# Kernel optimization log

Measured on AMD Instinct MI355X. Metric: run time of the kernel, lower is better.

Reference implementation:

```python
import jax, jax.numpy as jnp
import numpy as np

P = 2048
D = 1024
H = 16
DH = D // H
HID = 32


def setup_inputs() -> dict:
    key = jax.random.key(0)
    ks = jax.random.split(key, 10)
    s = 0.02
    return {
        "x": jax.random.normal(ks[0], (P, D), jnp.float32),
        "rel": jax.random.normal(ks[1], (P, P, 2), jnp.float32),
        "w_qkv": jax.random.normal(ks[2], (D, 3 * D), jnp.float32) * s,
        "w_proj": jax.random.normal(ks[3], (D, D), jnp.float32) * s,
        "rpb_w1": jax.random.normal(ks[4], (2, HID), jnp.float32) * s,
        "rpb_b1": jnp.zeros((HID,), jnp.float32),
        "rpb_w2": jax.random.normal(ks[5], (HID, HID), jnp.float32) * s,
        "rpb_b2": jnp.zeros((HID,), jnp.float32),
        "rpb_w3": jax.random.normal(ks[6], (HID, 1), jnp.float32) * s,
        "rpb_b3": jnp.zeros((1,), jnp.float32),
    }


def reference(x, rel, w_qkv, w_proj, rpb_w1, rpb_b1, rpb_w2, rpb_b2, rpb_w3, rpb_b3):
    scale = 1.0 / np.sqrt(DH)
    qkv = x @ w_qkv                                   # [P, 3D]
    q, k, v = jnp.split(qkv, 3, axis=-1)
    # [P, D] -> [H, P, DH]
    q = q.reshape(P, H, DH).transpose(1, 0, 2)
    k = k.reshape(P, H, DH).transpose(1, 0, 2)
    v = v.reshape(P, H, DH).transpose(1, 0, 2)
    logits = jnp.einsum('hpd,hqd->hpq', q, k) * scale  # [H, P, P]
    # RelPosBias MLP: (dx,dy) -> scalar, applied over [P, P, 2]
    hcur = jax.nn.relu(rel @ rpb_w1 + rpb_b1)
    hcur = jax.nn.relu(hcur @ rpb_w2 + rpb_b2)
    bias = (hcur @ rpb_w3 + rpb_b3)[..., 0]            # [P, P]
    logits = logits + bias[None]
    attn = jax.nn.softmax(logits, axis=-1)
    out = jnp.einsum('hpq,hqd->hpd', attn, v)          # [H, P, DH]
    out = out.transpose(1, 0, 2).reshape(P, D)
    return out @ w_proj
```

## Files before the change

### kernel.cpp

```cpp
#include <hip/hip_runtime.h>
#include <hip/hip_bf16.h>
#include <type_traits>

typedef __attribute__((ext_vector_type(8))) short bf16x8;
typedef __attribute__((ext_vector_type(4))) float floatx4;
typedef __attribute__((ext_vector_type(2))) float float2v;

__device__ __forceinline__ float bf2f(unsigned short u) {
    union { unsigned int x; float f; } v; v.x = ((unsigned int)u) << 16; return v.f;
}
__device__ __forceinline__ unsigned short f2bf(float f) {
    union { float f; unsigned int u; } v; v.f = f;
    unsigned int x = v.u;
    unsigned int r = x + 0x7fffu + ((x >> 16) & 1u);
    return (unsigned short)(r >> 16);
}

typedef const __attribute__((address_space(1))) unsigned int u32_g;
typedef __attribute__((address_space(3))) unsigned int u32_l;
__device__ __forceinline__ void gld_lds16(const void* g, void* l) {
    __builtin_amdgcn_global_load_lds((u32_g*)g, (u32_l*)l, 16, 0, 0);
}

__device__ __forceinline__ void trans32(const float* __restrict__ in,
                                        unsigned short* __restrict__ out,
                                        int K, int N, int bx, int by,
                                        unsigned short (*T)[33]) {
    const int n0 = bx * 32, k0 = by * 32;
    const int r = threadIdx.x >> 3;
    const int c4 = (threadIdx.x & 7) * 4;
    float4 v = *reinterpret_cast<const float4*>(in + (size_t)(k0 + r) * N + n0 + c4);
    T[c4 + 0][r] = f2bf(v.x);
    T[c4 + 1][r] = f2bf(v.y);
    T[c4 + 2][r] = f2bf(v.z);
    T[c4 + 3][r] = f2bf(v.w);
    __syncthreads();
    ushort4 o = {T[r][c4], T[r][c4 + 1], T[r][c4 + 2], T[r][c4 + 3]};
    *reinterpret_cast<ushort4*>(out + (size_t)(n0 + r) * K + k0 + c4) = o;
}

__global__ __launch_bounds__(256) void prep(const float* __restrict__ x,
                                            unsigned short* __restrict__ xb,
                                            const float* __restrict__ wq,
                                            unsigned short* __restrict__ wqT,
                                            const float* __restrict__ wp,
                                            unsigned short* __restrict__ wpT) {
    __shared__ unsigned short T[32][33];
    const int b = blockIdx.x;
    if (b < 1024) {
        size_t i = ((size_t)b * 256 + threadIdx.x) * 8;
        float4 a = *reinterpret_cast<const float4*>(x + i);
        float4 c = *reinterpret_cast<const float4*>(x + i + 4);
        unsigned short t[8] = {f2bf(a.x), f2bf(a.y), f2bf(a.z), f2bf(a.w),
                               f2bf(c.x), f2bf(c.y), f2bf(c.z), f2bf(c.w)};
        *reinterpret_cast<uint4*>(xb + i) = *reinterpret_cast<const uint4*>(t);
    } else if (b < 4096) {
        int t = b - 1024;
        trans32(wq, wqT, 1024, 3072, t % 96, t / 96, T);
    } else {
        int t = b - 4096;
        trans32(wp, wpT, 1024, 1024, t % 32, t / 32, T);
    }
}

__device__ __forceinline__ void gemm128_body(const unsigned short* __restrict__ A,
                                             const unsigned short* __restrict__ Bt,
                                             unsigned short* __restrict__ C,
                                             int bx, int by,
                                             unsigned short* __restrict__ S) {
    const int tid = threadIdx.x;
    const int wave = tid >> 6;
    const int lane = tid & 63;
    const int m15 = lane & 15;
    const int quad = lane >> 4;
    const int wm = wave >> 1;
    const int wn = wave & 1;
    const int m0 = by * 128;
    const int n0 = bx * 128;
    const int srow = lane >> 2;
    const int scol = (lane & 3) * 8;

    floatx4 acc[4][4];
#pragma unroll
    for (int mt = 0; mt < 4; mt++)
#pragma unroll
        for (int nt = 0; nt < 4; nt++) acc[mt][nt] = {0.f, 0.f, 0.f, 0.f};

    auto stage = [&](int k0, unsigned short* As, unsigned short* Bs) {
#pragma unroll
        for (int i = 0; i < 2; i++) {
            int j = wave * 2 + i;
            gld_lds16(A + (size_t)(m0 + j * 16 + srow) * 1024 + k0 + scol, &As[j * 16 * 32]);
            gld_lds16(Bt + (size_t)(n0 + j * 16 + srow) * 1024 + k0 + scol, &Bs[j * 16 * 32]);
        }
    };

    stage(0, S, S + 4096);
    __syncthreads();

    for (int kk = 0; kk < 32; ++kk) {
        unsigned short* As = S + (kk & 1) * 8192;
        unsigned short* Bs = As + 4096;
        if (kk < 31) {
            unsigned short* An = S + ((kk & 1) ^ 1) * 8192;
            stage((kk + 1) * 32, An, An + 4096);
        }

        bf16x8 a[4];
#pragma unroll
        for (int mt = 0; mt < 4; mt++)
            a[mt] = *reinterpret_cast<bf16x8*>(&As[(wm * 64 + mt * 16 + m15) * 32 + quad * 8]);
#pragma unroll
        for (int nt = 0; nt < 4; nt++) {
            bf16x8 b = *reinterpret_cast<bf16x8*>(&Bs[(wn * 64 + nt * 16 + m15) * 32 + quad * 8]);
#pragma unroll
            for (int mt = 0; mt < 4; mt++)
                acc[mt][nt] = __builtin_amdgcn_mfma_f32_16x16x32_bf16(a[mt], b, acc[mt][nt], 0, 0, 0);
        }
        __syncthreads();
    }

#pragma unroll
    for (int mt = 0; mt < 4; mt++)
#pragma unroll
        for (int nt = 0; nt < 4; nt++)
#pragma unroll
            for (int i = 0; i < 4; i++) {
                int row = m0 + wm * 64 + mt * 16 + quad * 4 + i;
                int col = n0 + wn * 64 + nt * 16 + m15;
                C[(size_t)row * 3072 + col] = f2bf(acc[mt][nt][i]);
            }
}

__device__ __forceinline__ void rpb_body(int bx,
                                         const float* __restrict__ rel,
                                         const float* __restrict__ w1,
                                         const float* __restrict__ b1,
                                         const float* __restrict__ w2,
                                         const float* __restrict__ b2,
                                         const float* __restrict__ w3,
                                         const float* __restrict__ b3,
                                         unsigned short* __restrict__ biasb) {
    const int tid = threadIdx.x;
    const int wave = tid >> 6;
    const int lane = tid & 63;
    const int m15 = lane & 15;
    const int quad = lane >> 4;

    bf16x8 af0, af1;
    {
        unsigned short t0[8], t1[8];
#pragma unroll
        for (int j = 0; j < 8; j++) {
            int k = quad * 8 + j;
            t0[j] = f2bf(w2[k * 32 + m15]);
            t1[j] = f2bf(w2[k * 32 + 16 + m15]);
        }
        af0 = *reinterpret_cast<bf16x8*>(t0);
        af1 = *reinterpret_cast<bf16x8*>(t1);
    }

    float2v w1a2[4], w1b2[4], b12[4];
#pragma unroll
    for (int p = 0; p < 4; p++) {
        int base = quad * 8 + 2 * p;
        w1a2[p] = {w1[base], w1[base + 1]};
        w1b2[p] = {w1[32 + base], w1[32 + base + 1]};
        b12[p]  = {b1[base], b1[base + 1]};
    }

    floatx4 b2r0, b2r1;
    float2v w3p00, w3p01, w3p10, w3p11;
    const float LOG2E = 1.44269504f;
    {
        float4 t0 = *reinterpret_cast<const float4*>(b2 + quad * 4);
        float4 t1 = *reinterpret_cast<const float4*>(b2 + 16 + quad * 4);
        b2r0 = {t0.x, t0.y, t0.z, t0.w};
        b2r1 = {t1.x, t1.y, t1.z, t1.w};
        float4 u0 = *reinterpret_cast<const float4*>(w3 + quad * 4);
        float4 u1 = *reinterpret_cast<const float4*>(w3 + 16 + quad * 4);
        w3p00 = {u0.x * LOG2E, u0.y * LOG2E};
        w3p01 = {u0.z * LOG2E, u0.w * LOG2E};
        w3p10 = {u1.x * LOG2E, u1.y * LOG2E};
        w3p11 = {u1.z * LOG2E, u1.w * LOG2E};
    }
    const float b3s = b3[0] * LOG2E;
    const float2v z2 = {0.f, 0.f};
    const floatx4 b3r = {b3s, b3s, b3s, b3s};

    bf16x8 sel;
    {
        unsigned short t[8];
#pragma unroll
        for (int j = 0; j < 8; j++)
            t[j] = (m15 == j) ? (unsigned short)0x3f80u : (unsigned short)0;
        sel = *reinterpret_cast<bf16x8*>(t);
    }

    const int base = bx * 1024 + wave * 64;

    float2 cur[4];
#pragma unroll
    for (int t = 0; t < 4; t++)
        cur[t] = *reinterpret_cast<const float2*>(rel + (size_t)(base + t * 16 + m15) * 2);

    for (int it = 0; it < 4; ++it) {
        const int pix0 = base + it * 256;
        float2 nxt[4];
        if (it < 3) {
#pragma unroll
            for (int t = 0; t < 4; t++)
                nxt[t] = *reinterpret_cast<const float2*>(rel + (size_t)(pix0 + 256 + t * 16 + m15) * 2);
        }

        float sreg[4];
#pragma unroll
        for (int t = 0; t < 4; t++) {
            float2v dx2 = {cur[t].x, cur[t].x}, dy2 = {cur[t].y, cur[t].y};

            unsigned int hp[4];
#pragma unroll
            for (int p = 0; p < 4; p++) {
                float2v h = __builtin_elementwise_fma(dx2, w1a2[p],
                             __builtin_elementwise_fma(dy2, w1b2[p], b12[p]));
                h = __builtin_elementwise_max(h, z2);
                hp[p] = __builtin_amdgcn_perm(__float_as_uint(h.y), __float_as_uint(h.x), 0x07060302u);
            }
            bf16x8 hb = *reinterpret_cast<bf16x8*>(hp);

            floatx4 d0 = __builtin_amdgcn_mfma_f32_16x16x32_bf16(af0, hb, b2r0, 0, 0, 0);
            floatx4 d1 = __builtin_amdgcn_mfma_f32_16x16x32_bf16(af1, hb, b2r1, 0, 0, 0);

            float2v m00 = __builtin_elementwise_max(__builtin_shufflevector(d0, d0, 0, 1), z2);
            float2v m01 = __builtin_elementwise_max(__builtin_shufflevector(d0, d0, 2, 3), z2);
            float2v m10 = __builtin_elementwise_max(__builtin_shufflevector(d1, d1, 0, 1), z2);
            float2v m11 = __builtin_elementwise_max(__builtin_shufflevector(d1, d1, 2, 3), z2);
            float2v acc2 = m00 * w3p00;
            acc2 = __builtin_elementwise_fma(m01, w3p01, acc2);
            acc2 = __builtin_elementwise_fma(m10, w3p10, acc2);
            acc2 = __builtin_elementwise_fma(m11, w3p11, acc2);
            sreg[t] = acc2.x + acc2.y;
        }

        unsigned int sb[4];
        sb[0] = (unsigned int)f2bf(sreg[0]) | ((unsigned int)f2bf(sreg[1]) << 16);
        sb[1] = (unsigned int)f2bf(sreg[2]) | ((unsigned int)f2bf(sreg[3]) << 16);
        sb[2] = 0; sb[3] = 0;
        bf16x8 sf = *reinterpret_cast<bf16x8*>(sb);
        floatx4 dsum = __builtin_amdgcn_mfma_f32_16x16x32_bf16(sel, sf, b3r, 0, 0, 0);

        if (quad == 0) {
            unsigned short o[4] = {f2bf(dsum[0]), f2bf(dsum[1]), f2bf(dsum[2]), f2bf(dsum[3])};
            *reinterpret_cast<ushort4*>(biasb + (size_t)pix0 + m15 * 4) =
                *reinterpret_cast<const ushort4*>(o);
        }

        if (it < 3) {
#pragma unroll
            for (int t = 0; t < 4; t++) cur[t] = nxt[t];
        }
    }
}

__global__ __launch_bounds__(256) void gemm_rpb(const unsigned short* __restrict__ xb,
                                                const unsigned short* __restrict__ wqT,
                                                unsigned short* __restrict__ qkv,
                                                const float* __restrict__ rel,
                                                const float* __restrict__ w1,
                                                const float* __restrict__ b1,
                                                const float* __restrict__ w2,
                                                const float* __restrict__ b2,
                                                const float* __restrict__ w3,
                                                const float* __restrict__ b3,
                                                unsigned short* __restrict__ biasb) {
    __shared__ __align__(16) unsigned short S[4 * 128 * 32];
    const int b = blockIdx.x;
    if (b < 384)
        gemm128_body(xb, wqT, qkv, b % 24, b / 24, S);
    else
        rpb_body(b - 384, rel, w1, b1, w2, b2, w3, b3, biasb);
}

template<int BN, typename TC>
__global__ __launch_bounds__(256) void gemm_abt(const unsigned short* __restrict__ A,
                                                const unsigned short* __restrict__ Bt,
                                                TC* __restrict__ C,
                                                int M, int N, int K) {
    constexpr int NT = BN / 32;
    __shared__ __align__(16) unsigned short As[2][64 * 32];
    __shared__ __align__(16) unsigned short Bs[2][BN * 32];

    const int tid = threadIdx.x;
    const int wave = tid >> 6;
    const int lane = tid & 63;
    const int m15 = lane & 15;
    const int quad = lane >> 4;
    const int wm = wave >> 1;
    const int wn = wave & 1;
    const int m0 = blockIdx.y * 64;
    const int n0 = blockIdx.x * BN;

    const int srow = lane >> 2;
    const int scol = (lane & 3) * 8;

    floatx4 acc[2][NT];
#pragma unroll
    for (int mt = 0; mt < 2; mt++)
#pragma unroll
        for (int nt = 0; nt < NT; nt++) acc[mt][nt] = {0.f, 0.f, 0.f, 0.f};

    auto stage = [&](int k0, int buf) {
        gld_lds16(A + (size_t)(m0 + wave * 16 + srow) * K + k0 + scol, &As[buf][wave * 16 * 32]);
#pragma unroll
        for (int i = 0; i < BN / 64; i++) {
            int j = wave * (BN / 64) + i;
            gld_lds16(Bt + (size_t)(n0 + j * 16 + srow) * K + k0 + scol, &Bs[buf][j * 16 * 32]);
        }
    };

    const int nk = K >> 5;
    stage(0, 0);
    __syncthreads();

    for (int kk = 0; kk < nk; ++kk) {
        const int cur = kk & 1;
        if (kk + 1 < nk) stage((kk + 1) * 32, cur ^ 1);

        bf16x8 a[2];
#pragma unroll
        for (int mt = 0; mt < 2; mt++)
            a[mt] = *reinterpret_cast<bf16x8*>(&As[cur][(wm * 32 + mt * 16 + m15) * 32 + quad * 8]);
#pragma unroll
        for (int nt = 0; nt < NT; nt++) {
            bf16x8 b = *reinterpret_cast<bf16x8*>(&Bs[cur][(wn * (BN / 2) + nt * 16 + m15) * 32 + quad * 8]);
#pragma unroll
            for (int mt = 0; mt < 2; mt++)
                acc[mt][nt] = __builtin_amdgcn_mfma_f32_16x16x32_bf16(a[mt], b, acc[mt][nt], 0, 0, 0);
        }
        __syncthreads();
    }

#pragma unroll
    for (int mt = 0; mt < 2; mt++)
#pragma unroll
        for (int nt = 0; nt < NT; nt++)
#pragma unroll
            for (int i = 0; i < 4; i++) {
                int row = m0 + wm * 32 + mt * 16 + quad * 4 + i;
                int col = n0 + wn * (BN / 2) + nt * 16 + m15;
                if constexpr (std::is_same<TC, float>::value)
                    C[(size_t)row * N + col] = acc[mt][nt][i];
                else
                    C[(size_t)row * N + col] = f2bf(acc[mt][nt][i]);
            }
}

__global__ __launch_bounds__(512, 4) void attn_kernel(const unsigned short* __restrict__ qkv,
                                                      const unsigned short* __restrict__ biasb,
                                                      unsigned short* __restrict__ attn_out) {
    const int h = blockIdx.x;
    const int q0 = blockIdx.y * 64;
    __shared__ __align__(16) unsigned short Kst[2][64 * 72];
    __shared__ __align__(16) unsigned short Vst[2][64 * 72];
    __shared__ __align__(16) unsigned short Ps[8][16 * 72];

    const int tid = threadIdx.x;
    const int g = tid >> 8;
    const int w = (tid >> 6) & 3;
    const int lane = tid & 63;
    const int ltid = tid & 255;
    const int m15 = lane & 15;
    const int quad = lane >> 4;

    bf16x8 qf[2];
#pragma unroll
    for (int kh = 0; kh < 2; kh++)
        qf[kh] = *reinterpret_cast<const bf16x8*>(
            qkv + (size_t)(q0 + w * 16 + m15) * 3072 + h * 64 + kh * 32 + quad * 8);

    const int kr0 = ltid >> 3, kd0 = (ltid & 7) * 8;
    const int ka = (ltid & 31) * 2;
    const int vd0 = (ltid >> 5) * 8;

    unsigned short* Kc = Kst[g];
    unsigned short* Vc = Vst[g];
    const size_t kofs = (size_t)g * 1024;

    uint4 kreg0 = *reinterpret_cast<const uint4*>(qkv + (kofs + kr0) * 3072 + 1024 + h * 64 + kd0);
    uint4 kreg1 = *reinterpret_cast<const uint4*>(qkv + (kofs + kr0 + 32) * 3072 + 1024 + h * 64 + kd0);
    uint4 vrega = *reinterpret_cast<const uint4*>(qkv + (kofs + ka) * 3072 + 2048 + h * 64 + vd0);
    uint4 vregb = *reinterpret_cast<const uint4*>(qkv + (kofs + ka + 1) * 3072 + 2048 + h * 64 + vd0);

    unsigned short br[16];
#pragma unroll
    for (int i = 0; i < 4; i++) {
        ushort4 t = *reinterpret_cast<const ushort4*>(
            biasb + (size_t)(q0 + w * 16 + quad * 4 + i) * 2048 + kofs + m15 * 4);
        br[0 * 4 + i] = t.x; br[1 * 4 + i] = t.y; br[2 * 4 + i] = t.z; br[3 * 4 + i] = t.w;
    }

    float rs[4] = {0.f, 0.f, 0.f, 0.f};
    floatx4 acc[4];
#pragma unroll
    for (int i = 0; i < 4; i++) acc[i] = {0.f, 0.f, 0.f, 0.f};
    const float c1 = 0.125f * 1.44269504f;

    for (int kt = 0; kt < 16; ++kt) {
        __syncthreads();

        *reinterpret_cast<uint4*>(&Kc[kr0 * 72 + kd0]) = kreg0;
        *reinterpret_cast<uint4*>(&Kc[(kr0 + 32) * 72 + kd0]) = kreg1;
        {
            const unsigned int* aw = reinterpret_cast<const unsigned int*>(&vrega);
            const unsigned int* bw = reinterpret_cast<const unsigned int*>(&vregb);
#pragma unroll
            for (int wd = 0; wd < 4; wd++) {
                unsigned int lo = __builtin_amdgcn_perm(bw[wd], aw[wd], 0x05040100u);
                unsigned int hi = __builtin_amdgcn_perm(bw[wd], aw[wd], 0x07060302u);
                *reinterpret_cast<unsigned int*>(&Vc[(vd0 + 2 * wd) * 72 + ka]) = lo;
                *reinterpret_cast<unsigned int*>(&Vc[(vd0 + 2 * wd + 1) * 72 + ka]) = hi;
            }
        }
        __syncthreads();

        if (kt < 15) {
            const size_t kb = kofs + (size_t)(kt + 1) * 64;
            kreg0 = *reinterpret_cast<const uint4*>(qkv + (kb + kr0) * 3072 + 1024 + h * 64 + kd0);
            kreg1 = *reinterpret_cast<const uint4*>(qkv + (kb + kr0 + 32) * 3072 + 1024 + h * 64 + kd0);
            vrega = *reinterpret_cast<const uint4*>(qkv + (kb + ka) * 3072 + 2048 + h * 64 + vd0);
            vregb = *reinterpret_cast<const uint4*>(qkv + (kb + ka + 1) * 3072 + 2048 + h * 64 + vd0);
        }

        floatx4 s[4];
#pragma unroll
        for (int nt = 0; nt < 4; nt++) s[nt] = {0.f, 0.f, 0.f, 0.f};
        __builtin_amdgcn_s_setprio(1);
#pragma unroll
        for (int kh = 0; kh < 2; kh++) {
#pragma unroll
            for (int nt = 0; nt < 4; nt++) {
                bf16x8 b = *reinterpret_cast<bf16x8*>(&Kc[(nt * 16 + m15) * 72 + kh * 32 + quad * 8]);
                s[nt] = __builtin_amdgcn_mfma_f32_16x16x32_bf16(qf[kh], b, s[nt], 0, 0, 0);
            }
        }
        __builtin_amdgcn_s_setprio(0);

        float p[4][4];
#pragma unroll
        for (int nt = 0; nt < 4; nt++)
#pragma unroll
            for (int i = 0; i < 4; i++) {
                float lg = fmaf(s[nt][i], c1, bf2f(br[nt * 4 + i]));
                p[nt][i] = __builtin_amdgcn_exp2f(lg);
                rs[i] += p[nt][i];
            }

        if (kt < 15) {
            const size_t kb = kofs + (size_t)(kt + 1) * 64;
#pragma unroll
            for (int i = 0; i < 4; i++) {
                ushort4 t = *reinterpret_cast<const ushort4*>(
                    biasb + (size_t)(q0 + w * 16 + quad * 4 + i) * 2048 + kb + m15 * 4);
                br[0 * 4 + i] = t.x; br[1 * 4 + i] = t.y; br[2 * 4 + i] = t.z; br[3 * 4 + i] = t.w;
            }
        }

        unsigned short* Pw = Ps[tid >> 6];
#pragma unroll
        for (int nt = 0; nt < 4; nt++)
#pragma unroll
            for (int i = 0; i < 4; i++)
                Pw[(quad * 4 + i) * 72 + nt * 16 + m15] = f2bf(p[nt][i]);
        __asm__ volatile("s_waitcnt lgkmcnt(0)" ::: "memory");

        __builtin_amdgcn_s_setprio(1);
#pragma unroll
        for (int kh = 0; kh < 2; kh++) {
            bf16x8 a = *reinterpret_cast<bf16x8*>(&Pw[m15 * 72 + kh * 32 + quad * 8]);
#pragma unroll
            for (int nt = 0; nt < 4; nt++) {
                bf16x8 b = *reinterpret_cast<bf16x8*>(&Vc[(nt * 16 + m15) * 72 + kh * 32 + quad * 8]);
                acc[nt] = __builtin_amdgcn_mfma_f32_16x16x32_bf16(a, b, acc[nt], 0, 0, 0);
            }
        }
        __builtin_amdgcn_s_setprio(0);
    }

    float rsum[4];
#pragma unroll
    for (int i = 0; i < 4; i++) {
        float r = rs[i];
        r += __shfl_xor(r, 1);
        r += __shfl_xor(r, 2);
        r += __shfl_xor(r, 4);
        r += __shfl_xor(r, 8);
        rsum[i] = r;
    }

    float* accbuf = reinterpret_cast<float*>(&Kst[0][0]);
    float* lbuf = accbuf + 4096;

    __syncthreads();
    if (g == 1) {
#pragma unroll
        for (int nt = 0; nt < 4; nt++)
#pragma unroll
            for (int i = 0; i < 4; i++)
                accbuf[(w * 16 + quad * 4 + i) * 64 + nt * 16 + m15] = acc[nt][i];
        if (m15 == 0) {
#pragma unroll
            for (int i = 0; i < 4; i++) lbuf[w * 16 + quad * 4 + i] = rsum[i];
        }
    }
    __syncthreads();
    if (g == 0) {
        float linv[4];
#pragma unroll
        for (int i = 0; i < 4; i++)
            linv[i] = 1.f / (rsum[i] + lbuf[w * 16 + quad * 4 + i]);
#pragma unroll
        for (int nt = 0; nt < 4; nt++)
#pragma unroll
            for (int i = 0; i < 4; i++) {
                float o = (acc[nt][i] + accbuf[(w * 16 + quad * 4 + i) * 64 + nt * 16 + m15]) * linv[i];
                int row = q0 + w * 16 + quad * 4 + i;
                int col = h * 64 + nt * 16 + m15;
                attn_out[(size_t)row * 1024 + col] = f2bf(o);
            }
    }
}

extern "C" void kernel_launch(void* const* d_in, const int* in_sizes, int n_in,
                              void* d_out, int out_size, void* d_ws, size_t ws_size,
                              hipStream_t stream) {
    const float* x      = (const float*)d_in[0];
    const float* rel    = (const float*)d_in[1];
    const float* w_qkv  = (const float*)d_in[2];
    const float* w_proj = (const float*)d_in[3];
    const float* w1     = (const float*)d_in[4];
    const float* b1     = (const float*)d_in[5];
    const float* w2     = (const float*)d_in[6];
    const float* b2     = (const float*)d_in[7];
    const float* w3     = (const float*)d_in[8];
    const float* b3     = (const float*)d_in[9];

    char* ws = (char*)d_ws;
    unsigned short* qkv   = (unsigned short*)ws;
    unsigned short* biasb = (unsigned short*)(ws + 12582912);
    unsigned short* xb    = (unsigned short*)(ws + 20971520);
    unsigned short* attn  = xb;
    unsigned short* wqT   = (unsigned short*)(ws + 25165824);
    unsigned short* wpT   = (unsigned short*)(ws + 31457280);
    float* out = (float*)d_out;

    prep<<<5120, 256, 0, stream>>>(x, xb, w_qkv, wqT, w_proj, wpT);
    gemm_rpb<<<4480, 256, 0, stream>>>(xb, wqT, qkv, rel, w1, b1, w2, b2, w3, b3, biasb);
    attn_kernel<<<dim3(16, 32), 512, 0, stream>>>(qkv, biasb, attn);
    gemm_abt<64, float><<<dim3(16, 32), 256, 0, stream>>>(attn, wpT, out, 2048, 1024, 1024);
}
```

Measured before the change: 208.8 us.

## Move RPB MLP into prep kernel and XOR-swizzle GEMM LDS tiles

```diff
diff --git a/kernel.cpp b/kernel.cpp
--- a/kernel.cpp
+++ b/kernel.cpp
@@ -39,27 +39,165 @@
     *reinterpret_cast<ushort4*>(out + (size_t)(n0 + r) * K + k0 + c4) = o;
 }
 
-__global__ __launch_bounds__(256) void prep(const float* __restrict__ x,
-                                            unsigned short* __restrict__ xb,
-                                            const float* __restrict__ wq,
-                                            unsigned short* __restrict__ wqT,
-                                            const float* __restrict__ wp,
-                                            unsigned short* __restrict__ wpT) {
+__device__ __forceinline__ void rpb_body(int bx,
+                                         const float* __restrict__ rel,
+                                         const float* __restrict__ w1,
+                                         const float* __restrict__ b1,
+                                         const float* __restrict__ w2,
+                                         const float* __restrict__ b2,
+                                         const float* __restrict__ w3,
+                                         const float* __restrict__ b3,
+                                         unsigned short* __restrict__ biasb) {
+    const int tid = threadIdx.x;
+    const int wave = tid >> 6;
+    const int lane = tid & 63;
+    const int m15 = lane & 15;
+    const int quad = lane >> 4;
+
+    bf16x8 af0, af1;
+    {
+        unsigned short t0[8], t1[8];
+#pragma unroll
+        for (int j = 0; j < 8; j++) {
+            int k = quad * 8 + j;
+            t0[j] = f2bf(w2[k * 32 + m15]);
+            t1[j] = f2bf(w2[k * 32 + 16 + m15]);
+        }
+        af0 = *reinterpret_cast<bf16x8*>(t0);
+        af1 = *reinterpret_cast<bf16x8*>(t1);
+    }
+
+    float2v w1a2[4], w1b2[4], b12[4];
+#pragma unroll
+    for (int p = 0; p < 4; p++) {
+        int base = quad * 8 + 2 * p;
+        w1a2[p] = {w1[base], w1[base + 1]};
+        w1b2[p] = {w1[32 + base], w1[32 + base + 1]};
+        b12[p]  = {b1[base], b1[base + 1]};
+    }
+
+    floatx4 b2r0, b2r1;
+    float2v w3p00, w3p01, w3p10, w3p11;
+    const float LOG2E = 1.44269504f;
+    {
+        float4 t0 = *reinterpret_cast<const float4*>(b2 + quad * 4);
+        float4 t1 = *reinterpret_cast<const float4*>(b2 + 16 + quad * 4);
+        b2r0 = {t0.x, t0.y, t0.z, t0.w};
+        b2r1 = {t1.x, t1.y, t1.z, t1.w};
+        float4 u0 = *reinterpret_cast<const float4*>(w3 + quad * 4);
+        float4 u1 = *reinterpret_cast<const float4*>(w3 + 16 + quad * 4);
+        w3p00 = {u0.x * LOG2E, u0.y * LOG2E};
+        w3p01 = {u0.z * LOG2E, u0.w * LOG2E};
+        w3p10 = {u1.x * LOG2E, u1.y * LOG2E};
+        w3p11 = {u1.z * LOG2E, u1.w * LOG2E};
+    }
+    const float b3s = b3[0] * LOG2E;
+    const float2v z2 = {0.f, 0.f};
+    const floatx4 b3r = {b3s, b3s, b3s, b3s};
+
+    bf16x8 sel;
+    {
+        unsigned short t[8];
+#pragma unroll
+        for (int j = 0; j < 8; j++)
+            t[j] = (m15 == j) ? (unsigned short)0x3f80u : (unsigned short)0;
+        sel = *reinterpret_cast<bf16x8*>(t);
+    }
+
+    const int base = bx * 1024 + wave * 64;
+
+    float2 cur[4];
+#pragma unroll
+    for (int t = 0; t < 4; t++)
+        cur[t] = *reinterpret_cast<const float2*>(rel + (size_t)(base + t * 16 + m15) * 2);
+
+    for (int it = 0; it < 4; ++it) {
+        const int pix0 = base + it * 256;
+        float2 nxt[4];
+        if (it < 3) {
+#pragma unroll
+            for (int t = 0; t < 4; t++)
+                nxt[t] = *reinterpret_cast<const float2*>(rel + (size_t)(pix0 + 256 + t * 16 + m15) * 2);
+        }
+
+        float sreg[4];
+#pragma unroll
+        for (int t = 0; t < 4; t++) {
+            float2v dx2 = {cur[t].x, cur[t].x}, dy2 = {cur[t].y, cur[t].y};
+
+            unsigned int hp[4];
+#pragma unroll
+            for (int p = 0; p < 4; p++) {
+                float2v h = __builtin_elementwise_fma(dx2, w1a2[p],
+                             __builtin_elementwise_fma(dy2, w1b2[p], b12[p]));
+                h = __builtin_elementwise_max(h, z2);
+                hp[p] = __builtin_amdgcn_perm(__float_as_uint(h.y), __float_as_uint(h.x), 0x07060302u);
+            }
+            bf16x8 hb = *reinterpret_cast<bf16x8*>(hp);
+
+            floatx4 d0 = __builtin_amdgcn_mfma_f32_16x16x32_bf16(af0, hb, b2r0, 0, 0, 0);
+            floatx4 d1 = __builtin_amdgcn_mfma_f32_16x16x32_bf16(af1, hb, b2r1, 0, 0, 0);
+
+            float2v m00 = __builtin_elementwise_max(__builtin_shufflevector(d0, d0, 0, 1), z2);
+            float2v m01 = __builtin_elementwise_max(__builtin_shufflevector(d0, d0, 2, 3), z2);
+            float2v m10 = __builtin_elementwise_max(__builtin_shufflevector(d1, d1, 0, 1), z2);
+            float2v m11 = __builtin_elementwise_max(__builtin_shufflevector(d1, d1, 2, 3), z2);
+            float2v acc2 = m00 * w3p00;
+            acc2 = __builtin_elementwise_fma(m01, w3p01, acc2);
+            acc2 = __builtin_elementwise_fma(m10, w3p10, acc2);
+            acc2 = __builtin_elementwise_fma(m11, w3p11, acc2);
+            sreg[t] = acc2.x + acc2.y;
+        }
+
+        unsigned int sb[4];
+        sb[0] = (unsigned int)f2bf(sreg[0]) | ((unsigned int)f2bf(sreg[1]) << 16);
+        sb[1] = (unsigned int)f2bf(sreg[2]) | ((unsigned int)f2bf(sreg[3]) << 16);
+        sb[2] = 0; sb[3] = 0;
+        bf16x8 sf = *reinterpret_cast<bf16x8*>(sb);
+        floatx4 dsum = __builtin_amdgcn_mfma_f32_16x16x32_bf16(sel, sf, b3r, 0, 0, 0);
+
+        if (quad == 0) {
+            unsigned short o[4] = {f2bf(dsum[0]), f2bf(dsum[1]), f2bf(dsum[2]), f2bf(dsum[3])};
+            *reinterpret_cast<ushort4*>(biasb + (size_t)pix0 + m15 * 4) =
+                *reinterpret_cast<const ushort4*>(o);
+        }
+
+        if (it < 3) {
+#pragma unroll
+            for (int t = 0; t < 4; t++) cur[t] = nxt[t];
+        }
+    }
+}
+
+__global__ __launch_bounds__(256, 4) void prep_rpb(
+        const float* __restrict__ x, unsigned short* __restrict__ xb,
+        const float* __restrict__ wq, unsigned short* __restrict__ wqT,
+        const float* __restrict__ wp, unsigned short* __restrict__ wpT,
+        const float* __restrict__ rel,
+        const float* __restrict__ w1, const float* __restrict__ b1,
+        const float* __restrict__ w2, const float* __restrict__ b2,
+        const float* __restrict__ w3, const float* __restrict__ b3,
+        unsigned short* __restrict__ biasb) {
     __shared__ unsigned short T[32][33];
     const int b = blockIdx.x;
-    if (b < 1024) {
-        size_t i = ((size_t)b * 256 + threadIdx.x) * 8;
+    if (b < 4096) {
+        rpb_body(b, rel, w1, b1, w2, b2, w3, b3, biasb);
+        return;
+    }
+    const int t = b - 4096;
+    if (t < 1024) {
+        size_t i = ((size_t)t * 256 + threadIdx.x) * 8;
         float4 a = *reinterpret_cast<const float4*>(x + i);
         float4 c = *reinterpret_cast<const float4*>(x + i + 4);
-        unsigned short t[8] = {f2bf(a.x), f2bf(a.y), f2bf(a.z), f2bf(a.w),
+        unsigned short u[8] = {f2bf(a.x), f2bf(a.y), f2bf(a.z), f2bf(a.w),
                                f2bf(c.x), f2bf(c.y), f2bf(c.z), f2bf(c.w)};
-        *reinterpret_cast<uint4*>(xb + i) = *reinterpret_cast<const uint4*>(t);
-    } else if (b < 4096) {
-        int t = b - 1024;
-        trans32(wq, wqT, 1024, 3072, t % 96, t / 96, T);
+        *reinterpret_cast<uint4*>(xb + i) = *reinterpret_cast<const uint4*>(u);
+    } else if (t < 4096) {
+        int u = t - 1024;
+        trans32(wq, wqT, 1024, 3072, u % 96, u / 96, T);
     } else {
-        int t = b - 4096;
-        trans32(wp, wpT, 1024, 1024, t % 32, t / 32, T);
+        int u = t - 4096;
+        trans32(wp, wpT, 1024, 1024, u % 32, u / 32, T);
     }
 }
 
@@ -78,7 +216,8 @@
     const int m0 = by * 128;
     const int n0 = bx * 128;
     const int srow = lane >> 2;
-    const int scol = (lane & 3) * 8;
+    const int scol = (((lane & 3) ^ ((lane >> 3) & 3)) * 8);
+    const int sw8 = (quad ^ ((m15 >> 1) & 3)) * 8;
 
     floatx4 acc[4][4];
 #pragma unroll
@@ -109,10 +248,10 @@
         bf16x8 a[4];
 #pragma unroll
         for (int mt = 0; mt < 4; mt++)
-            a[mt] = *reinterpret_cast<bf16x8*>(&As[(wm * 64 + mt * 16 + m15) * 32 + quad * 8]);
+            a[mt] = *reinterpret_cast<bf16x8*>(&As[(wm * 64 + mt * 16 + m15) * 32 + sw8]);
 #pragma unroll
         for (int nt = 0; nt < 4; nt++) {
-            bf16x8 b = *reinterpret_cast<bf16x8*>(&Bs[(wn * 64 + nt * 16 + m15) * 32 + quad * 8]);
+            bf16x8 b = *reinterpret_cast<bf16x8*>(&Bs[(wn * 64 + nt * 16 + m15) * 32 + sw8]);
 #pragma unroll
             for (int mt = 0; mt < 4; mt++)
                 acc[mt][nt] = __builtin_amdgcn_mfma_f32_16x16x32_bf16(a[mt], b, acc[mt][nt], 0, 0, 0);
@@ -132,153 +271,11 @@
             }
 }
 
-__device__ __forceinline__ void rpb_body(int bx,
-                                         const float* __restrict__ rel,
-                                         const float* __restrict__ w1,
-                                         const float* __restrict__ b1,
-                                         const float* __restrict__ w2,
-                                         const float* __restrict__ b2,
-                                         const float* __restrict__ w3,
-                                         const float* __restrict__ b3,
-                                         unsigned short* __restrict__ biasb) {
-    const int tid = threadIdx.x;
-    const int wave = tid >> 6;
-    const int lane = tid & 63;
-    const int m15 = lane & 15;
-    const int quad = lane >> 4;
-
-    bf16x8 af0, af1;
-    {
-        unsigned short t0[8], t1[8];
-#pragma unroll
-        for (int j = 0; j < 8; j++) {
-            int k = quad * 8 + j;
-            t0[j] = f2bf(w2[k * 32 + m15]);
-            t1[j] = f2bf(w2[k * 32 + 16 + m15]);
-        }
-        af0 = *reinterpret_cast<bf16x8*>(t0);
-        af1 = *reinterpret_cast<bf16x8*>(t1);
-    }
-
-    float2v w1a2[4], w1b2[4], b12[4];
-#pragma unroll
-    for (int p = 0; p < 4; p++) {
-        int base = quad * 8 + 2 * p;
-        w1a2[p] = {w1[base], w1[base + 1]};
-        w1b2[p] = {w1[32 + base], w1[32 + base + 1]};
-        b12[p]  = {b1[base], b1[base + 1]};
-    }
-
-    floatx4 b2r0, b2r1;
-    float2v w3p00, w3p01, w3p10, w3p11;
-    const float LOG2E = 1.44269504f;
-    {
-        float4 t0 = *reinterpret_cast<const float4*>(b2 + quad * 4);
-        float4 t1 = *reinterpret_cast<const float4*>(b2 + 16 + quad * 4);
-        b2r0 = {t0.x, t0.y, t0.z, t0.w};
-        b2r1 = {t1.x, t1.y, t1.z, t1.w};
-        float4 u0 = *reinterpret_cast<const float4*>(w3 + quad * 4);
-        float4 u1 = *reinterpret_cast<const float4*>(w3 + 16 + quad * 4);
-        w3p00 = {u0.x * LOG2E, u0.y * LOG2E};
-        w3p01 = {u0.z * LOG2E, u0.w * LOG2E};
-        w3p10 = {u1.x * LOG2E, u1.y * LOG2E};
-        w3p11 = {u1.z * LOG2E, u1.w * LOG2E};
-    }
-    const float b3s = b3[0] * LOG2E;
-    const float2v z2 = {0.f, 0.f};
-    const floatx4 b3r = {b3s, b3s, b3s, b3s};
-
-    bf16x8 sel;
-    {
-        unsigned short t[8];
-#pragma unroll
-        for (int j = 0; j < 8; j++)
-            t[j] = (m15 == j) ? (unsigned short)0x3f80u : (unsigned short)0;
-        sel = *reinterpret_cast<bf16x8*>(t);
-    }
-
-    const int base = bx * 1024 + wave * 64;
-
-    float2 cur[4];
-#pragma unroll
-    for (int t = 0; t < 4; t++)
-        cur[t] = *reinterpret_cast<const float2*>(rel + (size_t)(base + t * 16 + m15) * 2);
-
-    for (int it = 0; it < 4; ++it) {
-        const int pix0 = base + it * 256;
-        float2 nxt[4];
-        if (it < 3) {
-#pragma unroll
-            for (int t = 0; t < 4; t++)
-                nxt[t] = *reinterpret_cast<const float2*>(rel + (size_t)(pix0 + 256 + t * 16 + m15) * 2);
-        }
-
-        float sreg[4];
-#pragma unroll
-        for (int t = 0; t < 4; t++) {
-            float2v dx2 = {cur[t].x, cur[t].x}, dy2 = {cur[t].y, cur[t].y};
-
-            unsigned int hp[4];
-#pragma unroll
-            for (int p = 0; p < 4; p++) {
-                float2v h = __builtin_elementwise_fma(dx2, w1a2[p],
-                             __builtin_elementwise_fma(dy2, w1b2[p], b12[p]));
-                h = __builtin_elementwise_max(h, z2);
-                hp[p] = __builtin_amdgcn_perm(__float_as_uint(h.y), __float_as_uint(h.x), 0x07060302u);
-            }
-            bf16x8 hb = *reinterpret_cast<bf16x8*>(hp);
-
-            floatx4 d0 = __builtin_amdgcn_mfma_f32_16x16x32_bf16(af0, hb, b2r0, 0, 0, 0);
-            floatx4 d1 = __builtin_amdgcn_mfma_f32_16x16x32_bf16(af1, hb, b2r1, 0, 0, 0);
-
-            float2v m00 = __builtin_elementwise_max(__builtin_shufflevector(d0, d0, 0, 1), z2);
-            float2v m01 = __builtin_elementwise_max(__builtin_shufflevector(d0, d0, 2, 3), z2);
-            float2v m10 = __builtin_elementwise_max(__builtin_shufflevector(d1, d1, 0, 1), z2);
-            float2v m11 = __builtin_elementwise_max(__builtin_shufflevector(d1, d1, 2, 3), z2);
-            float2v acc2 = m00 * w3p00;
-            acc2 = __builtin_elementwise_fma(m01, w3p01, acc2);
-            acc2 = __builtin_elementwise_fma(m10, w3p10, acc2);
-            acc2 = __builtin_elementwise_fma(m11, w3p11, acc2);
-            sreg[t] = acc2.x + acc2.y;
-        }
-
-        unsigned int sb[4];
-        sb[0] = (unsigned int)f2bf(sreg[0]) | ((unsigned int)f2bf(sreg[1]) << 16);
-        sb[1] = (unsigned int)f2bf(sreg[2]) | ((unsigned int)f2bf(sreg[3]) << 16);
-        sb[2] = 0; sb[3] = 0;
-        bf16x8 sf = *reinterpret_cast<bf16x8*>(sb);
-        floatx4 dsum = __builtin_amdgcn_mfma_f32_16x16x32_bf16(sel, sf, b3r, 0, 0, 0);
-
-        if (quad == 0) {
-            unsigned short o[4] = {f2bf(dsum[0]), f2bf(dsum[1]), f2bf(dsum[2]), f2bf(dsum[3])};
-            *reinterpret_cast<ushort4*>(biasb + (size_t)pix0 + m15 * 4) =
-                *reinterpret_cast<const ushort4*>(o);
-        }
-
-        if (it < 3) {
-#pragma unroll
-            for (int t = 0; t < 4; t++) cur[t] = nxt[t];
-        }
-    }
-}
-
-__global__ __launch_bounds__(256) void gemm_rpb(const unsigned short* __restrict__ xb,
+__global__ __launch_bounds__(256) void gemm_qkv(const unsigned short* __restrict__ xb,
                                                 const unsigned short* __restrict__ wqT,
-                                                unsigned short* __restrict__ qkv,
-                                                const float* __restrict__ rel,
-                                                const float* __restrict__ w1,
-                                                const float* __restrict__ b1,
-                                                const float* __restrict__ w2,
-                                                const float* __restrict__ b2,
-                                                const float* __restrict__ w3,
-                                                const float* __restrict__ b3,
-                                                unsigned short* __restrict__ biasb) {
+                                                unsigned short* __restrict__ qkv) {
     __shared__ __align__(16) unsigned short S[4 * 128 * 32];
-    const int b = blockIdx.x;
-    if (b < 384)
-        gemm128_body(xb, wqT, qkv, b % 24, b / 24, S);
-    else
-        rpb_body(b - 384, rel, w1, b1, w2, b2, w3, b3, biasb);
+    gemm128_body(xb, wqT, qkv, blockIdx.x % 24, blockIdx.x / 24, S);
 }
 
 template<int BN, typename TC>
@@ -301,7 +298,8 @@
     const int n0 = blockIdx.x * BN;
 
     const int srow = lane >> 2;
-    const int scol = (lane & 3) * 8;
+    const int scol = (((lane & 3) ^ ((lane >> 3) & 3)) * 8);
+    const int sw8 = (quad ^ ((m15 >> 1) & 3)) * 8;
 
     floatx4 acc[2][NT];
 #pragma unroll
@@ -329,10 +327,10 @@
         bf16x8 a[2];
 #pragma unroll
         for (int mt = 0; mt < 2; mt++)
-            a[mt] = *reinterpret_cast<bf16x8*>(&As[cur][(wm * 32 + mt * 16 + m15) * 32 + quad * 8]);
+            a[mt] = *reinterpret_cast<bf16x8*>(&As[cur][(wm * 32 + mt * 16 + m15) * 32 + sw8]);
 #pragma unroll
         for (int nt = 0; nt < NT; nt++) {
-            bf16x8 b = *reinterpret_cast<bf16x8*>(&Bs[cur][(wn * (BN / 2) + nt * 16 + m15) * 32 + quad * 8]);
+            bf16x8 b = *reinterpret_cast<bf16x8*>(&Bs[cur][(wn * (BN / 2) + nt * 16 + m15) * 32 + sw8]);
 #pragma unroll
             for (int mt = 0; mt < 2; mt++)
                 acc[mt][nt] = __builtin_amdgcn_mfma_f32_16x16x32_bf16(a[mt], b, acc[mt][nt], 0, 0, 0);
@@ -553,8 +551,9 @@
     unsigned short* wpT   = (unsigned short*)(ws + 31457280);
     float* out = (float*)d_out;
 
-    prep<<<5120, 256, 0, stream>>>(x, xb, w_qkv, wqT, w_proj, wpT);
-    gemm_rpb<<<4480, 256, 0, stream>>>(xb, wqT, qkv, rel, w1, b1, w2, b2, w3, b3, biasb);
+    prep_rpb<<<9216, 256, 0, stream>>>(x, xb, w_qkv, wqT, w_proj, wpT,
+                                       rel, w1, b1, w2, b2, w3, b3, biasb);
+    gemm_qkv<<<384, 256, 0, stream>>>(xb, wqT, qkv);
     attn_kernel<<<dim3(16, 32), 512, 0, stream>>>(qkv, biasb, attn);
     gemm_abt<64, float><<<dim3(16, 32), 256, 0, stream>>>(attn, wpT, out, 2048, 1024, 1024);
 }
```

Result: slower. 215.0 us (+3.0%).

## Keep softmax probabilities in registers via transposed QK^T MFMA and permuted V layout

Applied to the files above, without the earlier changes.

```diff
diff --git a/kernel.cpp b/kernel.cpp
--- a/kernel.cpp
+++ b/kernel.cpp
@@ -14,6 +14,11 @@
     unsigned int x = v.u;
     unsigned int r = x + 0x7fffu + ((x >> 16) & 1u);
     return (unsigned short)(r >> 16);
+}
+__device__ __forceinline__ unsigned int pk2bf(float lo, float hi) {
+    float2 t; t.x = lo; t.y = hi;
+    __hip_bfloat162 h = __float22bfloat162_rn(t);
+    return *reinterpret_cast<unsigned int*>(&h);
 }
 
 typedef const __attribute__((address_space(1))) unsigned int u32_g;
@@ -355,14 +360,13 @@
             }
 }
 
-__global__ __launch_bounds__(512, 4) void attn_kernel(const unsigned short* __restrict__ qkv,
+__global__ __launch_bounds__(512, 6) void attn_kernel(const unsigned short* __restrict__ qkv,
                                                       const unsigned short* __restrict__ biasb,
                                                       unsigned short* __restrict__ attn_out) {
     const int h = blockIdx.x;
     const int q0 = blockIdx.y * 64;
     __shared__ __align__(16) unsigned short Kst[2][64 * 72];
     __shared__ __align__(16) unsigned short Vst[2][64 * 72];
-    __shared__ __align__(16) unsigned short Ps[8][16 * 72];
 
     const int tid = threadIdx.x;
     const int g = tid >> 8;
@@ -381,6 +385,7 @@
     const int kr0 = ltid >> 3, kd0 = (ltid & 7) * 8;
     const int ka = (ltid & 31) * 2;
     const int vd0 = (ltid >> 5) * 8;
+    const int ska = ((ka >> 5) & 1) * 32 + ((ka >> 2) & 3) * 8 + ((ka >> 4) & 1) * 4 + (ka & 3);
 
     unsigned short* Kc = Kst[g];
     unsigned short* Vc = Vst[g];
@@ -391,15 +396,14 @@
     uint4 vrega = *reinterpret_cast<const uint4*>(qkv + (kofs + ka) * 3072 + 2048 + h * 64 + vd0);
     uint4 vregb = *reinterpret_cast<const uint4*>(qkv + (kofs + ka + 1) * 3072 + 2048 + h * 64 + vd0);
 
-    unsigned short br[16];
-#pragma unroll
-    for (int i = 0; i < 4; i++) {
-        ushort4 t = *reinterpret_cast<const ushort4*>(
-            biasb + (size_t)(q0 + w * 16 + quad * 4 + i) * 2048 + kofs + m15 * 4);
-        br[0 * 4 + i] = t.x; br[1 * 4 + i] = t.y; br[2 * 4 + i] = t.z; br[3 * 4 + i] = t.w;
-    }
-
-    float rs[4] = {0.f, 0.f, 0.f, 0.f};
+    const unsigned short* bbase =
+        biasb + (size_t)(q0 + w * 16 + m15) * 2048 + kofs + quad * 16;
+    union BU { uint4 v[2]; unsigned short s[16]; };
+    BU br, nbr;
+    br.v[0] = *reinterpret_cast<const uint4*>(bbase);
+    br.v[1] = *reinterpret_cast<const uint4*>(bbase + 8);
+
+    float rs = 0.f;
     floatx4 acc[4];
 #pragma unroll
     for (int i = 0; i < 4; i++) acc[i] = {0.f, 0.f, 0.f, 0.f};
@@ -417,8 +421,8 @@
             for (int wd = 0; wd < 4; wd++) {
                 unsigned int lo = __builtin_amdgcn_perm(bw[wd], aw[wd], 0x05040100u);
                 unsigned int hi = __builtin_amdgcn_perm(bw[wd], aw[wd], 0x07060302u);
-                *reinterpret_cast<unsigned int*>(&Vc[(vd0 + 2 * wd) * 72 + ka]) = lo;
-                *reinterpret_cast<unsigned int*>(&Vc[(vd0 + 2 * wd + 1) * 72 + ka]) = hi;
+                *reinterpret_cast<unsigned int*>(&Vc[(vd0 + 2 * wd) * 72 + ska]) = lo;
+                *reinterpret_cast<unsigned int*>(&Vc[(vd0 + 2 * wd + 1) * 72 + ska]) = hi;
             }
         }
         __syncthreads();
@@ -431,71 +435,63 @@
             vregb = *reinterpret_cast<const uint4*>(qkv + (kb + ka + 1) * 3072 + 2048 + h * 64 + vd0);
         }
 
-        floatx4 s[4];
-#pragma unroll
-        for (int nt = 0; nt < 4; nt++) s[nt] = {0.f, 0.f, 0.f, 0.f};
+        floatx4 st[4];
+#pragma unroll
+        for (int nt = 0; nt < 4; nt++) st[nt] = {0.f, 0.f, 0.f, 0.f};
         __builtin_amdgcn_s_setprio(1);
 #pragma unroll
         for (int kh = 0; kh < 2; kh++) {
 #pragma unroll
             for (int nt = 0; nt < 4; nt++) {
-                bf16x8 b = *reinterpret_cast<bf16x8*>(&Kc[(nt * 16 + m15) * 72 + kh * 32 + quad * 8]);
-                s[nt] = __builtin_amdgcn_mfma_f32_16x16x32_bf16(qf[kh], b, s[nt], 0, 0, 0);
+                bf16x8 kb = *reinterpret_cast<bf16x8*>(&Kc[(nt * 16 + m15) * 72 + kh * 32 + quad * 8]);
+                st[nt] = __builtin_amdgcn_mfma_f32_16x16x32_bf16(kb, qf[kh], st[nt], 0, 0, 0);
             }
         }
         __builtin_amdgcn_s_setprio(0);
 
+        if (kt < 15) {
+            const unsigned short* nb = bbase + (size_t)(kt + 1) * 64;
+            nbr.v[0] = *reinterpret_cast<const uint4*>(nb);
+            nbr.v[1] = *reinterpret_cast<const uint4*>(nb + 8);
+        }
+
         float p[4][4];
 #pragma unroll
         for (int nt = 0; nt < 4; nt++)
 #pragma unroll
             for (int i = 0; i < 4; i++) {
-                float lg = fmaf(s[nt][i], c1, bf2f(br[nt * 4 + i]));
+                float lg = fmaf(st[nt][i], c1, bf2f(br.s[i * 4 + nt]));
                 p[nt][i] = __builtin_amdgcn_exp2f(lg);
-                rs[i] += p[nt][i];
-            }
-
-        if (kt < 15) {
-            const size_t kb = kofs + (size_t)(kt + 1) * 64;
-#pragma unroll
-            for (int i = 0; i < 4; i++) {
-                ushort4 t = *reinterpret_cast<const ushort4*>(
-                    biasb + (size_t)(q0 + w * 16 + quad * 4 + i) * 2048 + kb + m15 * 4);
-                br[0 * 4 + i] = t.x; br[1 * 4 + i] = t.y; br[2 * 4 + i] = t.z; br[3 * 4 + i] = t.w;
-            }
-        }
-
-        unsigned short* Pw = Ps[tid >> 6];
-#pragma unroll
-        for (int nt = 0; nt < 4; nt++)
-#pragma unroll
-            for (int i = 0; i < 4; i++)
-                Pw[(quad * 4 + i) * 72 + nt * 16 + m15] = f2bf(p[nt][i]);
-        __asm__ volatile("s_waitcnt lgkmcnt(0)" ::: "memory");
+                rs += p[nt][i];
+            }
+
+        bf16x8 paf[2];
+#pragma unroll
+        for (int kh = 0; kh < 2; kh++) {
+            unsigned int pw[4];
+            pw[0] = pk2bf(p[2 * kh][0], p[2 * kh][1]);
+            pw[1] = pk2bf(p[2 * kh][2], p[2 * kh][3]);
+            pw[2] = pk2bf(p[2 * kh + 1][0], p[2 * kh + 1][1]);
+            pw[3] = pk2bf(p[2 * kh + 1][2], p[2 * kh + 1][3]);
+            paf[kh] = *reinterpret_cast<bf16x8*>(pw);
+        }
 
         __builtin_amdgcn_s_setprio(1);
 #pragma unroll
         for (int kh = 0; kh < 2; kh++) {
-            bf16x8 a = *reinterpret_cast<bf16x8*>(&Pw[m15 * 72 + kh * 32 + quad * 8]);
 #pragma unroll
             for (int nt = 0; nt < 4; nt++) {
-                bf16x8 b = *reinterpret_cast<bf16x8*>(&Vc[(nt * 16 + m15) * 72 + kh * 32 + quad * 8]);
-                acc[nt] = __builtin_amdgcn_mfma_f32_16x16x32_bf16(a, b, acc[nt], 0, 0, 0);
+                bf16x8 vb = *reinterpret_cast<bf16x8*>(&Vc[(nt * 16 + m15) * 72 + kh * 32 + quad * 8]);
+                acc[nt] = __builtin_amdgcn_mfma_f32_16x16x32_bf16(paf[kh], vb, acc[nt], 0, 0, 0);
             }
         }
         __builtin_amdgcn_s_setprio(0);
-    }
-
-    float rsum[4];
-#pragma unroll
-    for (int i = 0; i < 4; i++) {
-        float r = rs[i];
-        r += __shfl_xor(r, 1);
-        r += __shfl_xor(r, 2);
-        r += __shfl_xor(r, 4);
-        r += __shfl_xor(r, 8);
-        rsum[i] = r;
-    }
+
+        if (kt < 15) { br.v[0] = nbr.v[0]; br.v[1] = nbr.v[1]; }
+    }
+
+    rs += __shfl_xor(rs, 16);
+    rs += __shfl_xor(rs, 32);
 
     float* accbuf = reinterpret_cast<float*>(&Kst[0][0]);
     float* lbuf = accbuf + 4096;
@@ -507,17 +503,15 @@
 #pragma unroll
             for (int i = 0; i < 4; i++)
                 accbuf[(w * 16 + quad * 4 + i) * 64 + nt * 16 + m15] = acc[nt][i];
-        if (m15 == 0) {
-#pragma unroll
-            for (int i = 0; i < 4; i++) lbuf[w * 16 + quad * 4 + i] = rsum[i];
-        }
+        if (lane < 16) lbuf[w * 16 + m15] = rs;
     }
     __syncthreads();
     if (g == 0) {
+        float rq = rs + lbuf[w * 16 + m15];
         float linv[4];
 #pragma unroll
         for (int i = 0; i < 4; i++)
-            linv[i] = 1.f / (rsum[i] + lbuf[w * 16 + quad * 4 + i]);
+            linv[i] = 1.f / __shfl(rq, quad * 4 + i);
 #pragma unroll
         for (int nt = 0; nt < 4; nt++)
 #pragma unroll
```

Result: slower. 273.4 us (+30.9%).
